# Kernel tuning notes

Measured on AMD Instinct MI355X. Metric: run time of the kernel, lower is better.

The kernel has to match this reference:

```python
import jax, jax.numpy as jnp
import numpy as np

RES = 64      # resolution (D=H=W)
WIDTH = 32    # FNO channel width
MODES = 8     # retained Fourier modes per dim
NL = 4        # FNO layers
NU = 0.000185 # viscosity
FCH = 128     # projection hidden width
B = 4


def setup_inputs() -> dict:
    key = jax.random.key(0)
    ks = jax.random.split(key, 8)
    u = jax.random.normal(ks[0], (B, 3, RES, RES, RES), jnp.float32)
    s = 1.0 / (WIDTH * WIDTH)
    fc0_w = jax.random.normal(ks[1], (3, WIDTH), jnp.float32) * (1.0 / 3.0) ** 0.5
    fc0_b = jnp.zeros((WIDTH,), jnp.float32)
    # (layer, corner, in, out, m1, m2, m3, re/im)
    spec_w = jax.random.normal(ks[2], (NL, 4, WIDTH, WIDTH, MODES, MODES, MODES, 2), jnp.float32) * s
    w_pw = jax.random.normal(ks[3], (NL, WIDTH, WIDTH), jnp.float32) * (1.0 / WIDTH) ** 0.5
    b_pw = jnp.zeros((NL, WIDTH), jnp.float32)
    fc1_w = jax.random.normal(ks[4], (WIDTH, FCH), jnp.float32) * (1.0 / WIDTH) ** 0.5
    fc1_b = jnp.zeros((FCH,), jnp.float32)
    fc2_w = jax.random.normal(ks[5], (FCH, 6), jnp.float32) * (1.0 / FCH) ** 0.5
    fc2_b = jnp.zeros((6,), jnp.float32)
    return dict(u=u, fc0_w=fc0_w, fc0_b=fc0_b, spec_w=spec_w, w_pw=w_pw,
                b_pw=b_pw, fc1_w=fc1_w, fc1_b=fc1_b, fc2_w=fc2_w, fc2_b=fc2_b)


def _pointwise(x, w, b):
    # 1x1x1 conv: (B,C,D,H,W) x (C,O) -> (B,O,D,H,W)
    return jnp.einsum('bcdhw,co->bodhw', x, w) + b[None, :, None, None, None]


def _spectral_conv(x, wf):
    m = MODES
    Bn, C, D, H, W = x.shape
    ft = jnp.fft.rfftn(x, axes=(-3, -2, -1))           # (B,C,D,H,W//2+1) complex64
    w = wf[..., 0] + 1j * wf[..., 1]                   # (4,C,O,m,m,m)
    mul = lambda blk, ww: jnp.einsum('bixyz,ioxyz->boxyz', blk, ww)
    out = jnp.zeros((Bn, w.shape[2], D, H, W // 2 + 1), jnp.complex64)
    out = out.at[:, :, :m, :m, :m].set(mul(ft[:, :, :m, :m, :m], w[0]))
    out = out.at[:, :, -m:, :m, :m].set(mul(ft[:, :, -m:, :m, :m], w[1]))
    out = out.at[:, :, :m, -m:, :m].set(mul(ft[:, :, :m, -m:, :m], w[2]))
    out = out.at[:, :, -m:, -m:, :m].set(mul(ft[:, :, -m:, -m:, :m], w[3]))
    return jnp.fft.irfftn(out, s=(D, H, W), axes=(-3, -2, -1))


def _fno(u, fc0_w, fc0_b, spec_w, w_pw, b_pw, fc1_w, fc1_b, fc2_w, fc2_b):
    x = _pointwise(u, fc0_w, fc0_b)
    for l in range(NL):
        x1 = _spectral_conv(x, spec_w[l])
        x2 = _pointwise(x, w_pw[l], b_pw[l])
        x = x1 + x2
        if l < NL - 1:
            x = jax.nn.gelu(x)
    x = jax.nn.gelu(_pointwise(x, fc1_w, fc1_b))
    return _pointwise(x, fc2_w, fc2_b)


def _ns_hard_core(u):
    # du/dt = -(u.grad)u + nu * lap(u), periodic central differences
    dx = 2.0 * np.pi / RES
    conv = jnp.zeros_like(u)
    diff = jnp.zeros_like(u)
    for j in range(3):
        ax = 2 + j
        up = jnp.roll(u, -1, axis=ax)
        um = jnp.roll(u, 1, axis=ax)
        du = (up - um) / (2.0 * dx)          # d u_i / d x_j for all i
        conv = conv - u[:, j:j + 1] * du
        diff = diff + (up - 2.0 * u + um) / (dx * dx)
    return conv + NU * diff


def reference(u, fc0_w, fc0_b, spec_w, w_pw, b_pw, fc1_w, fc1_b, fc2_w, fc2_b):
    du_hard = _ns_hard_core(u)
    tau = _fno(u, fc0_w, fc0_b, spec_w, w_pw, b_pw, fc1_w, fc1_b, fc2_w, fc2_b)
    du_dt = du_hard + tau[:, :3] * 0.001
    return du_dt, tau
```

## Files before the change

kernel.cpp:

```cpp
#include <hip/hip_runtime.h>
#include <hip/hip_bf16.h>

#define RES 64
#define WIDTH 32
#define MODES 8
#define R3 262144
#define TWO_PI_OVER_64 0.09817477042468103f

__device__ __forceinline__ float geluf(float x) {
    float g = 1.5957691216057308f * (x + 0.044715f * x * x * x);
    return x * __builtin_amdgcn_rcpf(1.0f + __expf(-g));
}

constexpr double tcos_(double x) {
    double r = 1.0, term = 1.0;
    for (int i = 1; i <= 12; i++) { term *= -x * x / ((2.0 * i - 1.0) * (2.0 * i)); r += term; }
    return r;
}
constexpr double tsin_(double x) {
    double r = x, term = x;
    for (int i = 1; i <= 12; i++) { term *= -x * x / ((2.0 * i) * (2.0 * i + 1.0)); r += term; }
    return r;
}
struct Tw64 { float c[64]; float s[64]; };
constexpr Tw64 mkTw() {
    Tw64 t{};
    const double th = 6.283185307179586476925286766559 / 64.0;
    for (int i = 0; i < 64; i++) {
        double a = th * (i <= 32 ? i : i - 64);
        t.c[i] = (float)tcos_(a);
        t.s[i] = (float)tsin_(a);
    }
    return t;
}
constexpr Tw64 TWT = mkTw();

__global__ void k_fc0(const float* __restrict__ u, const float* __restrict__ w,
                      const float* __restrict__ bias, float* __restrict__ X) {
    __shared__ float ws[96];
    __shared__ float bs[32];
    int t = threadIdx.x;
    if (t < 96) ws[t] = w[t];
    if (t < 32) bs[t] = bias[t];
    __syncthreads();
    size_t s = (size_t)blockIdx.x * 256 + t;
    int b = (int)(s >> 18);
    size_t p = s & (R3 - 1);
    const float* ub = u + (size_t)b * 3 * R3;
    float u0 = ub[p], u1 = ub[R3 + p], u2 = ub[2 * R3 + p];
    float* xb = X + (size_t)b * 32 * R3;
    #pragma unroll
    for (int o = 0; o < 32; o++) {
        xb[(size_t)o * R3 + p] = bs[o] + u0 * ws[o] + u1 * ws[32 + o] + u2 * ws[64 + o];
    }
}

__global__ void __launch_bounds__(256, 6)
k_fwd_zy(const float* __restrict__ X, float2* __restrict__ S2) {
    int t = threadIdx.x;
    int q = t >> 6, y = t & 63;
    int bcx0 = blockIdx.x * 4;
    __shared__ float2 zt[4][8][66];
    __shared__ float2 tw[64];
    if (t < 64) { float s, c; __sincosf(TWO_PI_OVER_64 * t, &s, &c); tw[t] = make_float2(c, s); }

    const float* row = X + (size_t)(bcx0 + q) * 4096 + (size_t)y * 64;
    float re[8], im[8];
    #pragma unroll
    for (int k = 0; k < 8; k++) { re[k] = 0.f; im[k] = 0.f; }
    #pragma unroll
    for (int zb = 0; zb < 8; zb++) {
        float xa[4], xb4[4];
        *(float4*)xa  = *(const float4*)(row + zb * 4);
        *(float4*)xb4 = *(const float4*)(row + zb * 4 + 32);
        #pragma unroll
        for (int j = 0; j < 4; j++) {
            int z = zb * 4 + j;
            float sv = xa[j] + xb4[j];
            float dv = xa[j] - xb4[j];
            #pragma unroll
            for (int k = 0; k < 8; k++) {
                float v = (k & 1) ? dv : sv;
                re[k] += v * TWT.c[(k * z) & 63];
                im[k] -= v * TWT.s[(k * z) & 63];
            }
        }
    }
    #pragma unroll
    for (int k = 0; k < 8; k++) zt[q][k][y] = make_float2(re[k], im[k]);
    __syncthreads();

    int l = t & 63;
    int jy = l >> 2, kp = l & 3;
    int f = jy < 8 ? jy : 48 + jy;
    int k0 = kp * 2;
    float re0 = 0.f, im0 = 0.f, re1 = 0.f, im1 = 0.f;
    #pragma unroll 8
    for (int yy = 0; yy < 64; yy++) {
        float2 w = tw[(f * yy) & 63];
        float2 v0 = zt[q][k0][yy];
        float2 v1 = zt[q][k0 + 1][yy];
        re0 += v0.x * w.x + v0.y * w.y;
        im0 += v0.y * w.x - v0.x * w.y;
        re1 += v1.x * w.x + v1.y * w.y;
        im1 += v1.y * w.x - v1.x * w.y;
    }
    float2* dst = S2 + (size_t)(bcx0 + q) * 128 + jy * 8 + k0;
    dst[0] = make_float2(re0, im0);
    dst[1] = make_float2(re1, im1);
}

__global__ void k_fwd_x(const float2* __restrict__ S2, float2* __restrict__ S3) {
    int bc = blockIdx.x >> 3, kz = blockIdx.x & 7;
    int t = threadIdx.x;
    __shared__ float2 in[64 * 16];
    __shared__ float2 tw[64];
    if (t < 64) { float s, c; __sincosf(TWO_PI_OVER_64 * t, &s, &c); tw[t] = make_float2(c, s); }
    #pragma unroll
    for (int i = 0; i < 4; i++) {
        int e = t + 256 * i;
        in[e] = S2[((size_t)bc * 1024 + e) * 8 + kz];
    }
    __syncthreads();
    int jx = t >> 4, jy = t & 15;
    int f = jx < 8 ? jx : 48 + jx;
    float re = 0.f, im = 0.f;
    for (int x = 0; x < 64; x++) {
        float2 v = in[x * 16 + jy];
        float2 w = tw[(f * x) & 63];
        re += v.x * w.x + v.y * w.y;
        im += v.y * w.x - v.x * w.y;
    }
    S3[(size_t)bc * 2048 + (size_t)t * 8 + kz] = make_float2(re, im);
}

__global__ void k_specmul(const float2* __restrict__ S3, const float* __restrict__ spec_w,
                          float2* __restrict__ S4, int layer) {
    int mp = blockIdx.x;
    int t = threadIdx.x;
    int jxy = mp >> 2;
    int kz0 = (mp & 3) * 2;
    int jy = jxy & 15, jx = jxy >> 4;
    int corner = (jx >= 8 ? 1 : 0) + (jy >= 8 ? 2 : 0);
    int m1 = jx & 7, m2 = jy & 7;
    int mode0 = jxy * 8 + kz0;
    __shared__ float4 W4[1024];
    __shared__ float2 inb[2][128];
    const float* wbase = spec_w + (size_t)layer * 4194304 + (size_t)corner * 1048576
                       + m1 * 128 + m2 * 16 + kz0 * 2;
    #pragma unroll
    for (int j = 0; j < 8; j++) {
        int e = t + 128 * j;
        int i = e >> 5, o = e & 31;
        W4[e] = *(const float4*)(wbase + (size_t)i * 32768 + (size_t)o * 1024);
    }
    inb[0][t] = S3[(size_t)t * 2048 + mode0];
    inb[1][t] = S3[(size_t)t * 2048 + mode0 + 1];
    __syncthreads();
    int b = t >> 5, o = t & 31;
    float re0 = 0.f, im0 = 0.f, re1 = 0.f, im1 = 0.f;
    #pragma unroll 8
    for (int i = 0; i < 32; i++) {
        float2 a0 = inb[0][b * 32 + i];
        float2 a1 = inb[1][b * 32 + i];
        float4 w = W4[i * 32 + o];
        re0 += a0.x * w.x - a0.y * w.y;
        im0 += a0.x * w.y + a0.y * w.x;
        re1 += a1.x * w.z - a1.y * w.w;
        im1 += a1.x * w.w + a1.y * w.z;
    }
    S4[(size_t)(b * 32 + o) * 2048 + mode0]     = make_float2(re0, im0);
    S4[(size_t)(b * 32 + o) * 2048 + mode0 + 1] = make_float2(re1, im1);
}

__global__ void k_inv_x(const float2* __restrict__ S4, float2* __restrict__ S5) {
    int bo = blockIdx.x >> 3, kz = blockIdx.x & 7;
    int t = threadIdx.x;
    __shared__ float2 in[256];
    __shared__ float2 tw[64];
    if (t < 64) { float s, c; __sincosf(TWO_PI_OVER_64 * t, &s, &c); tw[t] = make_float2(c, s); }
    in[t] = S4[(size_t)bo * 2048 + (size_t)t * 8 + kz];
    __syncthreads();
    int x = t & 63, g = t >> 6;
    #pragma unroll
    for (int m = 0; m < 4; m++) {
        int jy = g + 4 * m;
        float re = 0.f, im = 0.f;
        #pragma unroll
        for (int jx = 0; jx < 16; jx++) {
            int f = jx < 8 ? jx : 48 + jx;
            float2 v = in[jx * 16 + jy];
            float2 w = tw[(f * x) & 63];
            re += v.x * w.x - v.y * w.y;
            im += v.x * w.y + v.y * w.x;
        }
        S5[((size_t)bo * 64 + x) * 128 + jy * 8 + kz] = make_float2(re, im);
    }
}

__global__ void __launch_bounds__(256, 3)
k_inv_yz_pw(const float2* __restrict__ S5, const float* __restrict__ w_pw,
            const float* __restrict__ b_pw, float* __restrict__ X,
            int layer, int do_gelu) {
    int blk = blockIdx.x;
    int yg = blk & 7, x = (blk >> 3) & 63, b = blk >> 9;
    int t = threadIdx.x;
    __shared__ float2 s5s[32 * 132];
    __shared__ float2 st[256];
    __shared__ float xt[2048];
    __shared__ float2 tw[64];
    if (t < 64) { float s, c; __sincosf(TWO_PI_OVER_64 * t, &s, &c); tw[t] = make_float2(c, s); }
    #pragma unroll
    for (int i = 0; i < 8; i++) {
        int f4 = t + 256 * i;
        int o = f4 >> 6, j4 = f4 & 63;
        float4 v = ((const float4*)(S5 + ((size_t)(b * 32 + o) * 64 + x) * 128))[j4];
        *(float4*)(&s5s[o * 132 + j4 * 2]) = v;
    }
    size_t base0 = (size_t)b * 8388608 + (size_t)(x * 64 + yg * 8) * 64;
    float xr0, xr1, xr2, xr3, xr4, xr5, xr6, xr7;
    {
        const float* xp = X + base0 + (t & 63);
        int c0 = t >> 6;
        xr0 = xp[(size_t)(c0 +  0) * R3];
        xr1 = xp[(size_t)(c0 +  4) * R3];
        xr2 = xp[(size_t)(c0 +  8) * R3];
        xr3 = xp[(size_t)(c0 + 12) * R3];
        xr4 = xp[(size_t)(c0 + 16) * R3];
        xr5 = xp[(size_t)(c0 + 20) * R3];
        xr6 = xp[(size_t)(c0 + 24) * R3];
        xr7 = xp[(size_t)(c0 + 28) * R3];
    }
    __syncthreads();
    int z = t & 63, og = t >> 6;
    int og8 = og * 8;
    int og8u = __builtin_amdgcn_readfirstlane(og8);
    const float* wl = w_pw + layer * 1024 + og8u;
    const float* bl = b_pw + layer * 32 + og8u;
    float bt0 = bl[0], bt1 = bl[1], bt2 = bl[2], bt3 = bl[3];
    float bt4 = bl[4], bt5 = bl[5], bt6 = bl[6], bt7 = bl[7];
    float2 tz1 = tw[z];
    float2 tz2 = tw[(2 * z) & 63];
    float2 tz3 = tw[(3 * z) & 63];
    float2 tz4 = tw[(4 * z) & 63];
    float2 tz5 = tw[(5 * z) & 63];
    float2 tz6 = tw[(6 * z) & 63];
    float2 tz7 = tw[(7 * z) & 63];
    const float inv_n = 1.0f / 262144.0f;
    for (int yi = 0; yi < 8; yi++) {
        int y = yg * 8 + yi;
        size_t base = base0 + (size_t)yi * 64;
        {
            int e = t;
            xt[e +    0] = xr0; xt[e +  256] = xr1; xt[e +  512] = xr2; xt[e +  768] = xr3;
            xt[e + 1024] = xr4; xt[e + 1280] = xr5; xt[e + 1536] = xr6; xt[e + 1792] = xr7;
        }
        {
            int o = t >> 3, k = t & 7;
            float re = 0.f, im = 0.f;
            #pragma unroll
            for (int jy = 0; jy < 16; jy++) {
                int f = jy < 8 ? jy : 48 + jy;
                float2 v = s5s[o * 132 + jy * 8 + k];
                float2 w = tw[(f * y) & 63];
                re += v.x * w.x - v.y * w.y;
                im += v.x * w.y + v.y * w.x;
            }
            st[t] = make_float2(re, im);
        }
        __syncthreads();
        if (yi < 7) {
            const float* xp = X + base + 64 + (t & 63);
            int c0 = t >> 6;
            xr0 = xp[(size_t)(c0 +  0) * R3];
            xr1 = xp[(size_t)(c0 +  4) * R3];
            xr2 = xp[(size_t)(c0 +  8) * R3];
            xr3 = xp[(size_t)(c0 + 12) * R3];
            xr4 = xp[(size_t)(c0 + 16) * R3];
            xr5 = xp[(size_t)(c0 + 20) * R3];
            xr6 = xp[(size_t)(c0 + 24) * R3];
            xr7 = xp[(size_t)(c0 + 28) * R3];
        }
#define INVZ_S(o) (st[(o) * 8 + 0].x \
        + 2.f * (st[(o) * 8 + 1].x * tz1.x - st[(o) * 8 + 1].y * tz1.y) \
        + 2.f * (st[(o) * 8 + 2].x * tz2.x - st[(o) * 8 + 2].y * tz2.y) \
        + 2.f * (st[(o) * 8 + 3].x * tz3.x - st[(o) * 8 + 3].y * tz3.y) \
        + 2.f * (st[(o) * 8 + 4].x * tz4.x - st[(o) * 8 + 4].y * tz4.y) \
        + 2.f * (st[(o) * 8 + 5].x * tz5.x - st[(o) * 8 + 5].y * tz5.y) \
        + 2.f * (st[(o) * 8 + 6].x * tz6.x - st[(o) * 8 + 6].y * tz6.y) \
        + 2.f * (st[(o) * 8 + 7].x * tz7.x - st[(o) * 8 + 7].y * tz7.y))
        float acc0 = bt0 + INVZ_S(og8 + 0) * inv_n;
        float acc1 = bt1 + INVZ_S(og8 + 1) * inv_n;
        float acc2 = bt2 + INVZ_S(og8 + 2) * inv_n;
        float acc3 = bt3 + INVZ_S(og8 + 3) * inv_n;
        float acc4 = bt4 + INVZ_S(og8 + 4) * inv_n;
        float acc5 = bt5 + INVZ_S(og8 + 5) * inv_n;
        float acc6 = bt6 + INVZ_S(og8 + 6) * inv_n;
        float acc7 = bt7 + INVZ_S(og8 + 7) * inv_n;
#undef INVZ_S
        #pragma unroll 4
        for (int c = 0; c < 32; c++) {
            float xc = xt[c * 64 + z];
            const float* wr = wl + c * 32;
            float w0 = wr[0], w1 = wr[1], w2 = wr[2], w3 = wr[3];
            float w4 = wr[4], w5 = wr[5], w6 = wr[6], w7 = wr[7];
            acc0 += xc * w0; acc1 += xc * w1; acc2 += xc * w2; acc3 += xc * w3;
            acc4 += xc * w4; acc5 += xc * w5; acc6 += xc * w6; acc7 += xc * w7;
        }
        __syncthreads();
        float r;
        r = do_gelu ? geluf(acc0) : acc0; X[base + (size_t)(og8 + 0) * R3 + z] = r;
        r = do_gelu ? geluf(acc1) : acc1; X[base + (size_t)(og8 + 1) * R3 + z] = r;
        r = do_gelu ? geluf(acc2) : acc2; X[base + (size_t)(og8 + 2) * R3 + z] = r;
        r = do_gelu ? geluf(acc3) : acc3; X[base + (size_t)(og8 + 3) * R3 + z] = r;
        r = do_gelu ? geluf(acc4) : acc4; X[base + (size_t)(og8 + 4) * R3 + z] = r;
        r = do_gelu ? geluf(acc5) : acc5; X[base + (size_t)(og8 + 5) * R3 + z] = r;
        r = do_gelu ? geluf(acc6) : acc6; X[base + (size_t)(og8 + 6) * R3 + z] = r;
        r = do_gelu ? geluf(acc7) : acc7; X[base + (size_t)(og8 + 7) * R3 + z] = r;
    }
}

typedef short bf16x8_t __attribute__((ext_vector_type(8)));
typedef float f32x4_t __attribute__((ext_vector_type(4)));

__device__ __forceinline__ float dpp_add16(float v) {
    int i;
    i = __builtin_amdgcn_update_dpp(0, __builtin_bit_cast(int, v), 0xB1, 0xF, 0xF, true);
    v += __builtin_bit_cast(float, i);
    i = __builtin_amdgcn_update_dpp(0, __builtin_bit_cast(int, v), 0x4E, 0xF, 0xF, true);
    v += __builtin_bit_cast(float, i);
    i = __builtin_amdgcn_update_dpp(0, __builtin_bit_cast(int, v), 0x141, 0xF, 0xF, true);
    v += __builtin_bit_cast(float, i);
    i = __builtin_amdgcn_update_dpp(0, __builtin_bit_cast(int, v), 0x140, 0xF, 0xF, true);
    v += __builtin_bit_cast(float, i);
    return v;
}

__global__ void __launch_bounds__(256, 2)
k_head(const float* __restrict__ X, const float* __restrict__ w1,
       const float* __restrict__ b1, const float* __restrict__ w2,
       const float* __restrict__ b2, float* __restrict__ tau_out) {
    int t = threadIdx.x;
    int lane = t & 63;
    int wv = t >> 6;
    int m = lane & 15;
    int g = lane >> 4;
    size_t sblock = (size_t)blockIdx.x * 256;
    int b = (int)(sblock >> 18);
    size_t pblock = sblock & (R3 - 1);
    const float* xb = X + (size_t)b * 8388608 + pblock;

    bf16x8_t Bhi[8], Blo[8];
    #pragma unroll
    for (int tt = 0; tt < 8; tt++) {
        #pragma unroll
        for (int j = 0; j < 8; j++) {
            float w = w1[(g * 8 + j) * 128 + tt * 16 + m];
            unsigned bits = __builtin_bit_cast(unsigned, w);
            float hf = __builtin_bit_cast(float, bits & 0xFFFF0000u);
            float lof = w - hf;
            unsigned lb = __builtin_bit_cast(unsigned, lof);
            Bhi[tt][j] = (short)(bits >> 16);
            Blo[tt][j] = (short)(lb >> 16);
        }
    }
    float w2r[8][6];
    #pragma unroll
    for (int tt = 0; tt < 8; tt++)
        #pragma unroll
        for (int o = 0; o < 6; o++) w2r[tt][o] = w2[(tt * 16 + m) * 6 + o];
    float b1r[8];
    #pragma unroll
    for (int tt = 0; tt < 8; tt++) b1r[tt] = b1[tt * 16 + m];
    float b2m = b2[m < 6 ? m : 0];

    for (int it = 0; it < 4; it++) {
        int s16 = wv * 64 + it * 16;
        bf16x8_t Ahi, Alo;
        #pragma unroll
        for (int j = 0; j < 8; j++) {
            float xv = xb[(size_t)(g * 8 + j) * R3 + s16 + m];
            unsigned bits = __builtin_bit_cast(unsigned, xv);
            float hf = __builtin_bit_cast(float, bits & 0xFFFF0000u);
            float lof = xv - hf;
            unsigned lb = __builtin_bit_cast(unsigned, lof);
            Ahi[j] = (short)(bits >> 16);
            Alo[j] = (short)(lb >> 16);
        }
        float p0[6] = {0.f, 0.f, 0.f, 0.f, 0.f, 0.f};
        float p1[6] = {0.f, 0.f, 0.f, 0.f, 0.f, 0.f};
        float p2[6] = {0.f, 0.f, 0.f, 0.f, 0.f, 0.f};
        float p3[6] = {0.f, 0.f, 0.f, 0.f, 0.f, 0.f};
        #pragma unroll
        for (int tt = 0; tt < 8; tt++) {
            f32x4_t d = {0.f, 0.f, 0.f, 0.f};
            d = __builtin_amdgcn_mfma_f32_16x16x32_bf16(Ahi, Bhi[tt], d, 0, 0, 0);
            d = __builtin_amdgcn_mfma_f32_16x16x32_bf16(Ahi, Blo[tt], d, 0, 0, 0);
            d = __builtin_amdgcn_mfma_f32_16x16x32_bf16(Alo, Bhi[tt], d, 0, 0, 0);
            float a0 = geluf(d[0] + b1r[tt]);
            float a1 = geluf(d[1] + b1r[tt]);
            float a2 = geluf(d[2] + b1r[tt]);
            float a3 = geluf(d[3] + b1r[tt]);
            #pragma unroll
            for (int o = 0; o < 6; o++) {
                float w = w2r[tt][o];
                p0[o] += a0 * w; p1[o] += a1 * w; p2[o] += a2 * w; p3[o] += a3 * w;
            }
        }
        float q0 = 0.f, q1 = 0.f, q2 = 0.f, q3 = 0.f;
        #pragma unroll
        for (int o = 0; o < 6; o++) {
            float r0 = dpp_add16(p0[o]);
            float r1 = dpp_add16(p1[o]);
            float r2 = dpp_add16(p2[o]);
            float r3 = dpp_add16(p3[o]);
            q0 = (m == o) ? r0 : q0;
            q1 = (m == o) ? r1 : q1;
            q2 = (m == o) ? r2 : q2;
            q3 = (m == o) ? r3 : q3;
        }
        if (m < 6) {
            float4 vv = make_float4(q0 + b2m, q1 + b2m, q2 + b2m, q3 + b2m);
            *(float4*)(tau_out + (size_t)b * 6 * R3 + (size_t)m * R3 + pblock + s16 + g * 4) = vv;
        }
    }
}

__global__ void k_hard(const float* __restrict__ u, const float* __restrict__ tau,
                       float* __restrict__ out0) {
    size_t s = (size_t)blockIdx.x * 256 + threadIdx.x;
    int bi = (int)(s >> 18);
    int b = bi / 3, i = bi % 3;
    size_t p = s & (R3 - 1);
    int x = (int)(p >> 12), y = ((int)p >> 6) & 63, z = (int)p & 63;
    const float dx = TWO_PI_OVER_64;
    const float inv2dx = 1.0f / (2.0f * dx);
    const float invdx2 = 1.0f / (dx * dx);
    const float* ub = u + (size_t)b * 3 * R3;
    const float* ui = ub + (size_t)i * R3;
    int xp = (x + 1) & 63, xm = (x + 63) & 63;
    int yp = (y + 1) & 63, ym = (y + 63) & 63;
    int zp = (z + 1) & 63, zm = (z + 63) & 63;
    float c0 = ui[p];
    float upx = ui[((size_t)xp << 12) | (y << 6) | z], umx = ui[((size_t)xm << 12) | (y << 6) | z];
    float upy = ui[((size_t)x << 12) | (yp << 6) | z], umy = ui[((size_t)x << 12) | (ym << 6) | z];
    float upz = ui[((size_t)x << 12) | (y << 6) | zp], umz = ui[((size_t)x << 12) | (y << 6) | zm];
    float u0c = ub[p], u1c = ub[R3 + p], u2c = ub[2 * R3 + p];
    float conv = -(u0c * (upx - umx) + u1c * (upy - umy) + u2c * (upz - umz)) * inv2dx;
    float diff = (upx + umx + upy + umy + upz + umz - 6.0f * c0) * invdx2;
    float tauv = tau[(size_t)b * 6 * R3 + (size_t)i * R3 + p];
    out0[s] = conv + 0.000185f * diff + 0.001f * tauv;
}

extern "C" void kernel_launch(void* const* d_in, const int* in_sizes, int n_in,
                              void* d_out, int out_size, void* d_ws, size_t ws_size,
                              hipStream_t stream) {
    const float* u      = (const float*)d_in[0];
    const float* fc0_w  = (const float*)d_in[1];
    const float* fc0_b  = (const float*)d_in[2];
    const float* spec_w = (const float*)d_in[3];
    const float* w_pw   = (const float*)d_in[4];
    const float* b_pw   = (const float*)d_in[5];
    const float* fc1_w  = (const float*)d_in[6];
    const float* fc1_b  = (const float*)d_in[7];
    const float* fc2_w  = (const float*)d_in[8];
    const float* fc2_b  = (const float*)d_in[9];
    float* out = (float*)d_out;

    float* X = (float*)d_ws;

    float2* S2 = (float2*)(out);
    float2* S3 = (float2*)(out + 2097152);
    float2* S4 = (float2*)(out + 2621440);
    float2* S5 = (float2*)(out + 3145728);

    k_fc0<<<4096, 256, 0, stream>>>(u, fc0_w, fc0_b, X);

    for (int l = 0; l < 4; l++) {
        k_fwd_zy<<<2048, 256, 0, stream>>>(X, S2);
        k_fwd_x<<<1024, 256, 0, stream>>>(S2, S3);
        k_specmul<<<1024, 128, 0, stream>>>(S3, spec_w, S4, l);
        k_inv_x<<<1024, 256, 0, stream>>>(S4, S5);
        k_inv_yz_pw<<<2048, 256, 0, stream>>>(S5, w_pw, b_pw, X, l, (l < 3) ? 1 : 0);
    }

    float* tau_out = out + (size_t)4 * 3 * R3;
    k_head<<<4096, 256, 0, stream>>>(X, fc1_w, fc1_b, fc2_w, fc2_b, tau_out);
    k_hard<<<12288, 256, 0, stream>>>(u, tau_out, out);
}
```

Baseline: 1.057 ms.

## Fuse forward x-DFT, spectral mode multiply and inverse x-DFT into one kernel

Three kernels per layer (forward x-DFT, per-mode complex channel mixing, inverse x-DFT) are merged into one k_modes kernel, where each block handles one (batch, jy, kz) slice. The block does the x-transform, the channel mix and the inverse x-transform in shared memory, which removes the S3/S4 round trips and two launches per layer. k_fwd_zy now writes S2 in a transposed layout so each block can read its slice contiguously. In exchange, spectral weights are read straight from global memory with strided scalar loads instead of being staged as float4 in shared memory, and the grid shrinks to 512 blocks.

```diff
diff --git a/kernel.cpp b/kernel.cpp
--- a/kernel.cpp
+++ b/kernel.cpp
@@ -105,96 +105,79 @@
         re1 += v1.x * w.x + v1.y * w.y;
         im1 += v1.y * w.x - v1.x * w.y;
     }
-    float2* dst = S2 + (size_t)(bcx0 + q) * 128 + jy * 8 + k0;
-    dst[0] = make_float2(re0, im0);
-    dst[1] = make_float2(re1, im1);
-}
-
-__global__ void k_fwd_x(const float2* __restrict__ S2, float2* __restrict__ S3) {
-    int bc = blockIdx.x >> 3, kz = blockIdx.x & 7;
+    int plane = bcx0 + q;
+    int bc = plane >> 6, xx = plane & 63;
+    int bb = bc >> 5, cc = bc & 31;
+    float2* dst0 = S2 + ((size_t)((bb * 16 + jy) * 8 + k0)) * 2048 + cc * 64 + xx;
+    dst0[0]    = make_float2(re0, im0);
+    dst0[2048] = make_float2(re1, im1);
+}
+
+__global__ void __launch_bounds__(256, 2)
+k_modes(const float2* __restrict__ S2, const float* __restrict__ spec_w,
+        float2* __restrict__ S5, int layer) {
+    int blk = blockIdx.x;
+    int kz = blk & 7, jy = (blk >> 3) & 15, b = blk >> 7;
     int t = threadIdx.x;
-    __shared__ float2 in[64 * 16];
+    __shared__ float2 As[2048];
+    __shared__ float2 Fs[512];
+    __shared__ float2 Gs[512];
     __shared__ float2 tw[64];
     if (t < 64) { float s, c; __sincosf(TWO_PI_OVER_64 * t, &s, &c); tw[t] = make_float2(c, s); }
-    #pragma unroll
-    for (int i = 0; i < 4; i++) {
-        int e = t + 256 * i;
-        in[e] = S2[((size_t)bc * 1024 + e) * 8 + kz];
-    }
-    __syncthreads();
-    int jx = t >> 4, jy = t & 15;
-    int f = jx < 8 ? jx : 48 + jx;
-    float re = 0.f, im = 0.f;
-    for (int x = 0; x < 64; x++) {
-        float2 v = in[x * 16 + jy];
-        float2 w = tw[(f * x) & 63];
-        re += v.x * w.x + v.y * w.y;
-        im += v.y * w.x - v.x * w.y;
-    }
-    S3[(size_t)bc * 2048 + (size_t)t * 8 + kz] = make_float2(re, im);
-}
-
-__global__ void k_specmul(const float2* __restrict__ S3, const float* __restrict__ spec_w,
-                          float2* __restrict__ S4, int layer) {
-    int mp = blockIdx.x;
-    int t = threadIdx.x;
-    int jxy = mp >> 2;
-    int kz0 = (mp & 3) * 2;
-    int jy = jxy & 15, jx = jxy >> 4;
-    int corner = (jx >= 8 ? 1 : 0) + (jy >= 8 ? 2 : 0);
-    int m1 = jx & 7, m2 = jy & 7;
-    int mode0 = jxy * 8 + kz0;
-    __shared__ float4 W4[1024];
-    __shared__ float2 inb[2][128];
-    const float* wbase = spec_w + (size_t)layer * 4194304 + (size_t)corner * 1048576
-                       + m1 * 128 + m2 * 16 + kz0 * 2;
-    #pragma unroll
-    for (int j = 0; j < 8; j++) {
-        int e = t + 128 * j;
-        int i = e >> 5, o = e & 31;
-        W4[e] = *(const float4*)(wbase + (size_t)i * 32768 + (size_t)o * 1024);
-    }
-    inb[0][t] = S3[(size_t)t * 2048 + mode0];
-    inb[1][t] = S3[(size_t)t * 2048 + mode0 + 1];
-    __syncthreads();
-    int b = t >> 5, o = t & 31;
-    float re0 = 0.f, im0 = 0.f, re1 = 0.f, im1 = 0.f;
-    #pragma unroll 8
-    for (int i = 0; i < 32; i++) {
-        float2 a0 = inb[0][b * 32 + i];
-        float2 a1 = inb[1][b * 32 + i];
-        float4 w = W4[i * 32 + o];
-        re0 += a0.x * w.x - a0.y * w.y;
-        im0 += a0.x * w.y + a0.y * w.x;
-        re1 += a1.x * w.z - a1.y * w.w;
-        im1 += a1.x * w.w + a1.y * w.z;
-    }
-    S4[(size_t)(b * 32 + o) * 2048 + mode0]     = make_float2(re0, im0);
-    S4[(size_t)(b * 32 + o) * 2048 + mode0 + 1] = make_float2(re1, im1);
-}
-
-__global__ void k_inv_x(const float2* __restrict__ S4, float2* __restrict__ S5) {
-    int bo = blockIdx.x >> 3, kz = blockIdx.x & 7;
-    int t = threadIdx.x;
-    __shared__ float2 in[256];
-    __shared__ float2 tw[64];
-    if (t < 64) { float s, c; __sincosf(TWO_PI_OVER_64 * t, &s, &c); tw[t] = make_float2(c, s); }
-    in[t] = S4[(size_t)bo * 2048 + (size_t)t * 8 + kz];
-    __syncthreads();
-    int x = t & 63, g = t >> 6;
-    #pragma unroll
-    for (int m = 0; m < 4; m++) {
-        int jy = g + 4 * m;
+    const float2* s2b = S2 + (size_t)blk * 2048;
+    #pragma unroll
+    for (int i = 0; i < 4; i++)
+        ((float4*)As)[t + 256 * i] = ((const float4*)s2b)[t + 256 * i];
+    __syncthreads();
+    #pragma unroll
+    for (int i2 = 0; i2 < 2; i2++) {
+        int e = t + 256 * i2;
+        int c = e >> 4, jx = e & 15;
+        int f = jx < 8 ? jx : 48 + jx;
+        const float2* arow = As + c * 64;
+        float re = 0.f, im = 0.f;
+        for (int x = 0; x < 64; x++) {
+            float2 v = arow[x];
+            float2 w = tw[(f * x) & 63];
+            re += v.x * w.x + v.y * w.y;
+            im += v.y * w.x - v.x * w.y;
+        }
+        Fs[e] = make_float2(re, im);
+    }
+    __syncthreads();
+    #pragma unroll
+    for (int i2 = 0; i2 < 2; i2++) {
+        int e = t + 256 * i2;
+        int o = e >> 4, jx = e & 15;
+        int corner = (jx >= 8 ? 1 : 0) + (jy >= 8 ? 2 : 0);
+        const float* wb = spec_w + (size_t)layer * 4194304 + (size_t)corner * 1048576
+                        + (size_t)o * 1024 + (jx & 7) * 128 + (jy & 7) * 16 + kz * 2;
+        float re = 0.f, im = 0.f;
+        #pragma unroll 8
+        for (int i = 0; i < 32; i++) {
+            float2 a = Fs[i * 16 + jx];
+            const float* wp = wb + (size_t)i * 32768;
+            float wr = wp[0], wi = wp[1];
+            re += a.x * wr - a.y * wi;
+            im += a.x * wi + a.y * wr;
+        }
+        Gs[e] = make_float2(re, im);
+    }
+    __syncthreads();
+    #pragma unroll
+    for (int i2 = 0; i2 < 8; i2++) {
+        int e = t + 256 * i2;
+        int o = e >> 6, x = e & 63;
         float re = 0.f, im = 0.f;
         #pragma unroll
         for (int jx = 0; jx < 16; jx++) {
             int f = jx < 8 ? jx : 48 + jx;
-            float2 v = in[jx * 16 + jy];
+            float2 v = Gs[o * 16 + jx];
             float2 w = tw[(f * x) & 63];
             re += v.x * w.x - v.y * w.y;
             im += v.x * w.y + v.y * w.x;
         }
-        S5[((size_t)bo * 64 + x) * 128 + jy * 8 + kz] = make_float2(re, im);
+        S5[((size_t)(b * 32 + o) * 64 + x) * 128 + jy * 8 + kz] = make_float2(re, im);
     }
 }
 
@@ -470,17 +453,13 @@
     float* X = (float*)d_ws;
 
     float2* S2 = (float2*)(out);
-    float2* S3 = (float2*)(out + 2097152);
-    float2* S4 = (float2*)(out + 2621440);
     float2* S5 = (float2*)(out + 3145728);
 
     k_fc0<<<4096, 256, 0, stream>>>(u, fc0_w, fc0_b, X);
 
     for (int l = 0; l < 4; l++) {
         k_fwd_zy<<<2048, 256, 0, stream>>>(X, S2);
-        k_fwd_x<<<1024, 256, 0, stream>>>(S2, S3);
-        k_specmul<<<1024, 128, 0, stream>>>(S3, spec_w, S4, l);
-        k_inv_x<<<1024, 256, 0, stream>>>(S4, S5);
+        k_modes<<<512, 256, 0, stream>>>(S2, spec_w, S5, l);
         k_inv_yz_pw<<<2048, 256, 0, stream>>>(S5, w_pw, b_pw, X, l, (l < 3) ? 1 : 0);
     }
 
```

New measurement: 1.128 ms. +6.7%, slower.
